# Kernel tuning notes

Hardware: AMD Instinct MI355X
Metric: run time of the kernel (lower is better)

The kernel has to match this reference:

```python
import jax, jax.numpy as jnp
import numpy as np

H = 1024  # hidden_size
N = 2 * H # encoder feature dim


def setup_inputs() -> dict:
    key = jax.random.key(0)
    ks = jax.random.split(key, 8)
    T, B = 2048, 16
    dec = jax.random.normal(ks[0], (B, H), dtype=jnp.float32)
    enc = jax.random.normal(ks[1], (T, B, N), dtype=jnp.float32)
    mask = jax.random.randint(ks[2], (T, B), 0, 2) > 0
    cov = jax.random.uniform(ks[3], (T, B), dtype=jnp.float32)
    # parameters (PyTorch Linear convention: y = x @ W.T + b)
    Wd = jax.random.normal(ks[4], (N, H), dtype=jnp.float32) / np.sqrt(H)
    bd = jnp.zeros((N,), dtype=jnp.float32)
    wc = jax.random.normal(ks[5], (N,), dtype=jnp.float32)  # coverage_projection: Linear(1, N, bias=False)
    v = jax.random.normal(ks[6], (N,), dtype=jnp.float32) / np.sqrt(N)  # v: Linear(N, 1, bias=False)
    return {"decoder_hidden_states": dec, "encoder_outs": enc,
            "encoder_padding_mask": mask, "coverage": cov,
            "Wd": Wd, "bd": bd, "wc": wc, "v": v}


def reference(decoder_hidden_states, encoder_outs, encoder_padding_mask, coverage, Wd, bd, wc, v):
    # dec_fea: [B, N]
    dec_fea = decoder_hidden_states @ Wd.T + bd
    # att_features: [T, B, N] = enc + broadcast dec + coverage feature
    att = encoder_outs + dec_fea[None, :, :] + coverage[:, :, None] * wc[None, None, :]
    e = jnp.tanh(att)
    # attn_scores: [T, B] via matvec with v
    scores = jnp.einsum('tbn,n->tb', e, v)
    scores = jnp.where(encoder_padding_mask, -jnp.inf, scores)
    attn_dist = jax.nn.softmax(scores, axis=0)  # softmax over T
    # context: [B, N]
    c = jnp.einsum('tb,tbn->bn', attn_dist, encoder_outs)
    coverage_out = coverage + attn_dist
    return (c, attn_dist, coverage_out)
```

## Files before the change

kernel.cpp:

```cpp
#include <hip/hip_runtime.h>


#define HH 1024
#define NNF 2048
#define TTT 2048
#define BB 16
#define NCHUNK 64
#define NWCHUNK 256
#define RPW 8

#define WS_DECFEA 0
#define WS_P      (BB * NNF)
#define WS_LPART  (WS_P + TTT * BB)
#define WS_LINV   (WS_LPART + NWCHUNK * BB)
#define WS_CPART  (WS_LINV + 16)

__device__ __forceinline__ float tanh_fast(float x) {
    float e = __expf(2.0f * x);
    return 1.0f - 2.0f * __builtin_amdgcn_rcpf(e + 1.0f);
}

__global__ __launch_bounds__(256) void k_decfea(const float* __restrict__ dec,
                                                const float* __restrict__ Wd,
                                                const float* __restrict__ bd,
                                                float* __restrict__ dec_fea) {
    const int n    = (blockIdx.x * 256 + threadIdx.x) >> 6;
    const int lane = threadIdx.x & 63;
    const float* wr = Wd + (size_t)n * HH;

    float acc[BB];
#pragma unroll
    for (int b = 0; b < BB; ++b) acc[b] = 0.0f;

#pragma unroll
    for (int it = 0; it < 4; ++it) {
        const int h = it * 256 + lane * 4;
        const float4 w4 = *(const float4*)(wr + h);
#pragma unroll
        for (int b = 0; b < BB; ++b) {
            const float4 d4 = *(const float4*)(dec + b * HH + h);
            acc[b] = fmaf(w4.x, d4.x, acc[b]);
            acc[b] = fmaf(w4.y, d4.y, acc[b]);
            acc[b] = fmaf(w4.z, d4.z, acc[b]);
            acc[b] = fmaf(w4.w, d4.w, acc[b]);
        }
    }
#pragma unroll
    for (int b = 0; b < BB; ++b) {
#pragma unroll
        for (int off = 32; off; off >>= 1) acc[b] += __shfl_xor(acc[b], off, 64);
    }
    if (lane == 0) {
        const float bias = bd[n];
#pragma unroll
        for (int b = 0; b < BB; ++b) dec_fea[b * NNF + n] = acc[b] + bias;
    }
}

__global__ __launch_bounds__(256, 2) void k_main(const float* __restrict__ enc,
                                                 const int* __restrict__ mask,
                                                 const float* __restrict__ cov,
                                                 const float* __restrict__ wc,
                                                 const float* __restrict__ v,
                                                 float* __restrict__ ws) {
    const int b     = blockIdx.y;
    const int chunk = blockIdx.x;
    const int tid   = threadIdx.x;
    const int lane  = tid & 63;
    const int w     = tid >> 6;
    const int t0    = chunk * (4 * RPW) + w * RPW;
    const int nb    = lane * 4;

    const float* dec_fea = ws + WS_DECFEA;
    float* ws_p     = ws + WS_P;
    float* ws_lpart = ws + WS_LPART;
    float* cpart    = ws + WS_CPART;

    float4 d[8], wv[8], vv[8], c[8];
#pragma unroll
    for (int s = 0; s < 8; ++s) {
        const int n = s * 256 + nb;
        d[s]  = *(const float4*)(dec_fea + b * NNF + n);
        wv[s] = *(const float4*)(wc + n);
        vv[s] = *(const float4*)(v + n);
        c[s]  = make_float4(0.f, 0.f, 0.f, 0.f);
    }

    float l_loc = 0.0f;

    for (int r = 0; r < RPW; ++r) {
        const int t = t0 + r;
        const float* row = enc + ((size_t)t * BB + b) * NNF;
        float4 f[8];
#pragma unroll
        for (int s = 0; s < 8; ++s) f[s] = *(const float4*)(row + s * 256 + nb);
        const float cv = cov[t * BB + b];

        float sa = 0.0f;
#pragma unroll
        for (int s = 0; s < 8; ++s) {
            float a;
            a = fmaf(cv, wv[s].x, f[s].x + d[s].x); sa = fmaf(tanh_fast(a), vv[s].x, sa);
            a = fmaf(cv, wv[s].y, f[s].y + d[s].y); sa = fmaf(tanh_fast(a), vv[s].y, sa);
            a = fmaf(cv, wv[s].z, f[s].z + d[s].z); sa = fmaf(tanh_fast(a), vv[s].z, sa);
            a = fmaf(cv, wv[s].w, f[s].w + d[s].w); sa = fmaf(tanh_fast(a), vv[s].w, sa);
        }
#pragma unroll
        for (int off = 32; off; off >>= 1) sa += __shfl_xor(sa, off, 64);

        const bool pad = mask[t * BB + b] != 0;
        const float p = pad ? 0.0f : __expf(sa);
        l_loc += p;
#pragma unroll
        for (int s = 0; s < 8; ++s) {
            c[s].x = fmaf(p, f[s].x, c[s].x);
            c[s].y = fmaf(p, f[s].y, c[s].y);
            c[s].z = fmaf(p, f[s].z, c[s].z);
            c[s].w = fmaf(p, f[s].w, c[s].w);
        }
        if (lane == 0) ws_p[t * BB + b] = p;
    }

    const int wchunk = chunk * 4 + w;
    if (lane == 0) ws_lpart[wchunk * BB + b] = l_loc;
    float* cp = cpart + (size_t)(wchunk * BB + b) * NNF;
#pragma unroll
    for (int s = 0; s < 8; ++s) *(float4*)(cp + s * 256 + nb) = c[s];
}

__global__ __launch_bounds__(256) void k_linv(float* __restrict__ ws) {
    __shared__ float lds[256];
    const int tid = threadIdx.x;
    const int b  = tid & (BB - 1);
    const int j0 = tid >> 4;
    float s = 0.0f;
#pragma unroll
    for (int jj = 0; jj < 16; ++jj) s += ws[WS_LPART + (j0 * 16 + jj) * BB + b];
    lds[tid] = s;
    __syncthreads();
    if (tid < BB) {
        float tot = 0.0f;
#pragma unroll
        for (int k = 0; k < 16; ++k) tot += lds[k * BB + tid];
        ws[WS_LINV + tid] = 1.0f / tot;
    }
}

__global__ __launch_bounds__(256) void k_finc(const float* __restrict__ ws,
                                              float* __restrict__ out_c) {
    const int gid  = blockIdx.x * 256 + threadIdx.x;
    const int idx4 = gid * 4;
    const int b = idx4 >> 11;
    const int n = idx4 & (NNF - 1);
    float4 s = {0.f, 0.f, 0.f, 0.f};
    for (int j = 0; j < NWCHUNK; ++j) {
        const float4 a = *(const float4*)(ws + WS_CPART + (size_t)(j * BB + b) * NNF + n);
        s.x += a.x; s.y += a.y; s.z += a.z; s.w += a.w;
    }
    const float li = ws[WS_LINV + b];
    s.x *= li; s.y *= li; s.z *= li; s.w *= li;
    *(float4*)(out_c + idx4) = s;
}

__global__ __launch_bounds__(256) void k_fina(const float* __restrict__ ws,
                                              const float* __restrict__ cov,
                                              float* __restrict__ out_attn,
                                              float* __restrict__ out_cov) {
    const int idx = blockIdx.x * 256 + threadIdx.x;
    const int b = idx & (BB - 1);
    const float a = ws[WS_P + idx] * ws[WS_LINV + b];
    out_attn[idx] = a;
    out_cov[idx] = cov[idx] + a;
}

extern "C" void kernel_launch(void* const* d_in, const int* in_sizes, int n_in,
                              void* d_out, int out_size, void* d_ws, size_t ws_size,
                              hipStream_t stream) {
    const float* dec  = (const float*)d_in[0];
    const float* enc  = (const float*)d_in[1];
    const int*   mask = (const int*)d_in[2];
    const float* cov  = (const float*)d_in[3];
    const float* Wd   = (const float*)d_in[4];
    const float* bd   = (const float*)d_in[5];
    const float* wc   = (const float*)d_in[6];
    const float* v    = (const float*)d_in[7];
    float* ws  = (float*)d_ws;
    float* out = (float*)d_out;

    float* out_c    = out;
    float* out_attn = out + BB * NNF;
    float* out_cov  = out_attn + TTT * BB;

    k_decfea<<<512, 256, 0, stream>>>(dec, Wd, bd, ws + WS_DECFEA);

    dim3 g2(NCHUNK, BB);
    k_main<<<g2, 256, 0, stream>>>(enc, mask, cov, wc, v, ws);

    k_linv<<<1, 256, 0, stream>>>(ws);

    k_finc<<<32, 256, 0, stream>>>(ws, out_c);

    k_fina<<<128, 256, 0, stream>>>(ws, cov, out_attn, out_cov);
}
```

Before: 419.4 us.

## Reduce context partials in LDS, prefetch rows, fuse finalize kernels

The main kernel now sums the four per-wave context partials in shared memory before writing, so it writes one partial per block and cuts partial-buffer traffic fourfold. It also software-prefetches the next encoder row into registers while the current row is processed. The separate normalizer, context-reduction and attention finalize kernels are merged into one launch, and each block recomputes the softmax normalizers. This adds LDS use and register pressure in the main kernel, and the normalizer sum is repeated in every finalize block.

```diff
diff --git a/kernel.cpp b/kernel.cpp
--- a/kernel.cpp
+++ b/kernel.cpp
@@ -6,14 +6,12 @@
 #define TTT 2048
 #define BB 16
 #define NCHUNK 64
-#define NWCHUNK 256
 #define RPW 8
 
 #define WS_DECFEA 0
 #define WS_P      (BB * NNF)
 #define WS_LPART  (WS_P + TTT * BB)
-#define WS_LINV   (WS_LPART + NWCHUNK * BB)
-#define WS_CPART  (WS_LINV + 16)
+#define WS_CPART  (WS_LPART + NCHUNK * BB)
 
 __device__ __forceinline__ float tanh_fast(float x) {
     float e = __expf(2.0f * x);
@@ -88,12 +86,22 @@
 
     float l_loc = 0.0f;
 
+    float4 f[8];
+    {
+        const float* row = enc + ((size_t)t0 * BB + b) * NNF;
+#pragma unroll
+        for (int s = 0; s < 8; ++s) f[s] = *(const float4*)(row + s * 256 + nb);
+    }
+
+#pragma unroll
     for (int r = 0; r < RPW; ++r) {
         const int t = t0 + r;
-        const float* row = enc + ((size_t)t * BB + b) * NNF;
-        float4 f[8];
-#pragma unroll
-        for (int s = 0; s < 8; ++s) f[s] = *(const float4*)(row + s * 256 + nb);
+        float4 fn[8];
+        if (r + 1 < RPW) {
+            const float* rowN = enc + ((size_t)(t + 1) * BB + b) * NNF;
+#pragma unroll
+            for (int s = 0; s < 8; ++s) fn[s] = *(const float4*)(rowN + s * 256 + nb);
+        }
         const float cv = cov[t * BB + b];
 
         float sa = 0.0f;
@@ -119,58 +127,82 @@
             c[s].w = fmaf(p, f[s].w, c[s].w);
         }
         if (lane == 0) ws_p[t * BB + b] = p;
-    }
-
-    const int wchunk = chunk * 4 + w;
-    if (lane == 0) ws_lpart[wchunk * BB + b] = l_loc;
-    float* cp = cpart + (size_t)(wchunk * BB + b) * NNF;
-#pragma unroll
-    for (int s = 0; s < 8; ++s) *(float4*)(cp + s * 256 + nb) = c[s];
-}
-
-__global__ __launch_bounds__(256) void k_linv(float* __restrict__ ws) {
-    __shared__ float lds[256];
+#pragma unroll
+        for (int s = 0; s < 8; ++s) f[s] = fn[s];
+    }
+
+    __shared__ float cbuf[4][NNF];
+    __shared__ float lred[4];
+#pragma unroll
+    for (int s = 0; s < 8; ++s) *(float4*)(&cbuf[w][s * 256 + nb]) = c[s];
+    if (lane == 0) lred[w] = l_loc;
+    __syncthreads();
+
+    float* cp = cpart + (size_t)(chunk * BB + b) * NNF;
+#pragma unroll
+    for (int half = 0; half < 2; ++half) {
+        const int e = half * 1024 + tid * 4;
+        float4 s0 = *(const float4*)(&cbuf[0][e]);
+        float4 s1 = *(const float4*)(&cbuf[1][e]);
+        float4 s2 = *(const float4*)(&cbuf[2][e]);
+        float4 s3 = *(const float4*)(&cbuf[3][e]);
+        float4 o;
+        o.x = (s0.x + s1.x) + (s2.x + s3.x);
+        o.y = (s0.y + s1.y) + (s2.y + s3.y);
+        o.z = (s0.z + s1.z) + (s2.z + s3.z);
+        o.w = (s0.w + s1.w) + (s2.w + s3.w);
+        *(float4*)(cp + e) = o;
+    }
+    if (tid == 0)
+        ws_lpart[chunk * BB + b] = (lred[0] + lred[1]) + (lred[2] + lred[3]);
+}
+
+__global__ __launch_bounds__(256) void k_fin(const float* __restrict__ ws,
+                                             const float* __restrict__ cov,
+                                             float* __restrict__ out_c,
+                                             float* __restrict__ out_attn,
+                                             float* __restrict__ out_cov) {
     const int tid = threadIdx.x;
-    const int b  = tid & (BB - 1);
-    const int j0 = tid >> 4;
-    float s = 0.0f;
-#pragma unroll
-    for (int jj = 0; jj < 16; ++jj) s += ws[WS_LPART + (j0 * 16 + jj) * BB + b];
-    lds[tid] = s;
+    __shared__ float pr[16][17];
+    __shared__ float linv[16];
+    {
+        const int bb = tid & 15;
+        const int g  = tid >> 4;
+        float s = 0.0f;
+#pragma unroll
+        for (int k = 0; k < 4; ++k)
+            s += ws[WS_LPART + (g * 4 + k) * BB + bb];
+        pr[g][bb] = s;
+    }
     __syncthreads();
-    if (tid < BB) {
+    if (tid < 16) {
         float tot = 0.0f;
 #pragma unroll
-        for (int k = 0; k < 16; ++k) tot += lds[k * BB + tid];
-        ws[WS_LINV + tid] = 1.0f / tot;
-    }
-}
-
-__global__ __launch_bounds__(256) void k_finc(const float* __restrict__ ws,
-                                              float* __restrict__ out_c) {
-    const int gid  = blockIdx.x * 256 + threadIdx.x;
-    const int idx4 = gid * 4;
-    const int b = idx4 >> 11;
-    const int n = idx4 & (NNF - 1);
-    float4 s = {0.f, 0.f, 0.f, 0.f};
-    for (int j = 0; j < NWCHUNK; ++j) {
-        const float4 a = *(const float4*)(ws + WS_CPART + (size_t)(j * BB + b) * NNF + n);
-        s.x += a.x; s.y += a.y; s.z += a.z; s.w += a.w;
-    }
-    const float li = ws[WS_LINV + b];
-    s.x *= li; s.y *= li; s.z *= li; s.w *= li;
-    *(float4*)(out_c + idx4) = s;
-}
-
-__global__ __launch_bounds__(256) void k_fina(const float* __restrict__ ws,
-                                              const float* __restrict__ cov,
-                                              float* __restrict__ out_attn,
-                                              float* __restrict__ out_cov) {
-    const int idx = blockIdx.x * 256 + threadIdx.x;
-    const int b = idx & (BB - 1);
-    const float a = ws[WS_P + idx] * ws[WS_LINV + b];
-    out_attn[idx] = a;
-    out_cov[idx] = cov[idx] + a;
+        for (int g = 0; g < 16; ++g) tot += pr[g][tid];
+        linv[tid] = 1.0f / tot;
+    }
+    __syncthreads();
+
+    if (blockIdx.x < 32) {
+        const int k = blockIdx.x;
+        const int b = k >> 1;
+        const int n = (k & 1) * 1024 + tid * 4;
+        float4 s = {0.f, 0.f, 0.f, 0.f};
+#pragma unroll 8
+        for (int j = 0; j < NCHUNK; ++j) {
+            const float4 a = *(const float4*)(ws + WS_CPART + (size_t)(j * BB + b) * NNF + n);
+            s.x += a.x; s.y += a.y; s.z += a.z; s.w += a.w;
+        }
+        const float li = linv[b];
+        s.x *= li; s.y *= li; s.z *= li; s.w *= li;
+        *(float4*)(out_c + b * NNF + n) = s;
+    } else {
+        const int idx = (blockIdx.x - 32) * 256 + tid;
+        const int b = idx & (BB - 1);
+        const float a = ws[WS_P + idx] * linv[b];
+        out_attn[idx] = a;
+        out_cov[idx] = cov[idx] + a;
+    }
 }
 
 extern "C" void kernel_launch(void* const* d_in, const int* in_sizes, int n_in,
@@ -196,9 +228,5 @@
     dim3 g2(NCHUNK, BB);
     k_main<<<g2, 256, 0, stream>>>(enc, mask, cov, wc, v, ws);
 
-    k_linv<<<1, 256, 0, stream>>>(ws);
-
-    k_finc<<<32, 256, 0, stream>>>(ws, out_c);
-
-    k_fina<<<128, 256, 0, stream>>>(ws, cov, out_attn, out_cov);
-}
+    k_fin<<<160, 256, 0, stream>>>(ws, cov, out_c, out_attn, out_cov);
+}
```

Result: slower. 436.5 us (+4.1%).
